# Kernel optimization log

Hardware: AMD Instinct MI355X
Metric: run time of the kernel (lower is better)

The kernel has to match this reference:

```python
import jax, jax.numpy as jnp
import numpy as np

N_NODES = 10000
W_DIM = 512
N_EDGES = 200000


def setup_inputs() -> dict:
    key = jax.random.key(0)
    k1, k2, k3 = jax.random.split(key, 3)
    z_drug = jax.random.normal(k1, (N_NODES, W_DIM), dtype=jnp.float32)
    # glorot-style init for the bilinear weight
    glorot_std = jnp.sqrt(2.0 / (W_DIM + W_DIM)).astype(jnp.float32)
    weight = jax.random.normal(k2, (W_DIM, W_DIM), dtype=jnp.float32) * glorot_std
    batch_edges = jax.random.randint(k3, (2, N_EDGES), 0, N_NODES, dtype=jnp.int64)
    return {"z_drug": z_drug, "weight": weight, "batch_edges": batch_edges}


def reference(z_drug, weight, batch_edges):
    # edge_type == 'drug_drug': both endpoints come from the drug table.
    row_embed = z_drug[batch_edges[0]]  # [E, d]
    col_embed = z_drug[batch_edges[1]]  # [E, d]
    # score_e = row_e @ W @ col_e  == diag((Z1 W) Z2^T) without the N x N blowup
    score = jnp.einsum('ed,df,ef->e', row_embed, weight, col_embed)
    return jax.nn.sigmoid(score)  # is_sigmoid=True default
```

## Files before the change

kernel.cpp:

```cpp
#include <hip/hip_runtime.h>
#include <math.h>

#define DIM     512
#define NNODES  10000
#define NEDGES  200000
#define MPAD    10240
#define NMB     160
#define NGRP    5
#define NB      (NGRP * NNODES)
#define SCAN_N  49
#define GEMM_GRID (NMB * 4)

#define HIST_BLK   50
#define SCAN_BASE  50
#define SCAT_BASE  99
#define SCAT_N     98
#define GEMM_BASE  197
#define FUSE_GRID  (GEMM_BASE + GEMM_GRID)

using floatx4 = __attribute__((ext_vector_type(4))) float;
using half8   = __attribute__((ext_vector_type(8))) _Float16;
using half2v  = __attribute__((ext_vector_type(2))) _Float16;

template <int N> struct IC { static constexpr int v = N; };

__device__ inline float dot2acc(half2v a, half2v b, float c) {
#if __has_builtin(__builtin_amdgcn_fdot2)
    return __builtin_amdgcn_fdot2(a, b, c, false);
#else
    return fmaf((float)a[0], (float)b[0], fmaf((float)a[1], (float)b[1], c));
#endif
}

__device__ inline int aload(const int* p) {
    return __hip_atomic_load(p, __ATOMIC_RELAXED, __HIP_MEMORY_SCOPE_AGENT);
}
__device__ inline void astore(int* p, int v) {
    __hip_atomic_store(p, v, __ATOMIC_RELAXED, __HIP_MEMORY_SCOPE_AGENT);
}
__device__ inline void waitflag(int* f, int target) {
    while (__hip_atomic_load(f, __ATOMIC_RELAXED, __HIP_MEMORY_SCOPE_AGENT) < target)
        __builtin_amdgcn_s_sleep(8);
    __atomic_signal_fence(__ATOMIC_ACQUIRE);
}
__device__ inline void signal(int* f) {
    __atomic_signal_fence(__ATOMIC_RELEASE);
    __hip_atomic_fetch_add(f, 1, __ATOMIC_RELAXED, __HIP_MEMORY_SCOPE_AGENT);
}

#define PREP_ZBLK 2560
__global__ __launch_bounds__(256) void prep(const float* __restrict__ Z,
                                            const float* __restrict__ W,
                                            _Float16* __restrict__ Zh16,
                                            _Float16* __restrict__ Wh16t,
                                            int* __restrict__ counts,
                                            int* __restrict__ flags) {
    const int b = blockIdx.x;
    const int t = threadIdx.x;

    if (b == 0 && t < 4) flags[t] = 0;

    if (b < 196) {
        int i = b * 256 + t;
        if (i < NB) counts[i] = 0;
    }

    if (b < PREP_ZBLK) {
        const int idx8 = (b * 256 + t) * 8;
        const int m = idx8 >> 9;
        float x[8];
        if (m < NNODES) {
            float4 v0 = *(const float4*)(Z + idx8);
            float4 v1 = *(const float4*)(Z + idx8 + 4);
            x[0]=v0.x; x[1]=v0.y; x[2]=v0.z; x[3]=v0.w;
            x[4]=v1.x; x[5]=v1.y; x[6]=v1.z; x[7]=v1.w;
        } else {
            #pragma unroll
            for (int j = 0; j < 8; ++j) x[j] = 0.f;
        }
        half8 h;
        #pragma unroll
        for (int j = 0; j < 8; ++j) h[j] = (_Float16)x[j];
        *(half8*)(Zh16 + idx8) = h;
    } else {
        __shared__ float tile[64][65];
        const int wb = b - PREP_ZBLK;
        const int kb = (wb >> 3) * 64;
        const int nb = (wb & 7) * 64;
        const int kk = t >> 2;
        const int ch = t & 3;

        const float* src = W + (size_t)(kb + kk) * DIM + nb + ch * 16;
        #pragma unroll
        for (int q = 0; q < 4; ++q) {
            float4 v = *(const float4*)(src + q * 4);
            tile[kk][ch * 16 + q * 4 + 0] = v.x;
            tile[kk][ch * 16 + q * 4 + 1] = v.y;
            tile[kk][ch * 16 + q * 4 + 2] = v.z;
            tile[kk][ch * 16 + q * 4 + 3] = v.w;
        }
        __syncthreads();

        const int nn = kk;
        half8 h0, h1;
        #pragma unroll
        for (int i = 0; i < 8; ++i) h0[i] = (_Float16)tile[ch * 16 + i][nn];
        #pragma unroll
        for (int i = 0; i < 8; ++i) h1[i] = (_Float16)tile[ch * 16 + 8 + i][nn];
        _Float16* d = Wh16t + (size_t)(nb + nn) * DIM + kb + ch * 16;
        *(half8*)(d)     = h0;
        *(half8*)(d + 8) = h1;
    }
}

__global__ __launch_bounds__(256, 3) void gemm_sort(
        const _Float16* __restrict__ Zh16,
        const _Float16* __restrict__ Wh16t,
        _Float16* __restrict__ ZWh,
        const int* __restrict__ eidx,
        int* __restrict__ counts,
        int* __restrict__ cursor,
        int* __restrict__ blksum,
        unsigned* __restrict__ keys,
        unsigned short* __restrict__ rows16,
        int* __restrict__ flags)
{
    __shared__ _Float16 Abuf[2][2 * 64 * 32];
    __shared__ _Float16 Bbuf[2][2 * 128 * 32];
    __shared__ int wsum[4];
    __shared__ int sbase;

    const int t   = threadIdx.x;
    const int bid = blockIdx.x;

    if (bid >= GEMM_BASE) {
        const int s8  = bid - GEMM_BASE;
        const int cxd = bid & 7;
        const int rr  = s8 >> 3;
        const int mg  = (rr >> 2) * 8 + cxd;
        const int m0  = mg * 64;
        const int n0  = (rr & 3) * 128;

        const int l  = t & 63;
        const int w  = t >> 6;
        const int wn = w * 32;
        const int lm = l & 15;
        const int lq = l >> 4;
        const unsigned wbase = (unsigned)(t & 192);

        floatx4 acc[4][2] = {};

        auto stage = [&](int buf, int k0) {
            #pragma unroll
            for (int p = 0; p < 2; ++p) {
                const int s   = p * 256 + t;
                const int kk  = s >> 8;
                const int row = (s >> 2) & 63;
                const int ch  = s & 3;
                const _Float16* src = Zh16 + (size_t)(m0 + row) * DIM + k0 + kk * 32 + ch * 8;
                __builtin_amdgcn_global_load_lds(
                    (const __attribute__((address_space(1))) void*)src,
                    (__attribute__((address_space(3))) void*)&Abuf[buf][(p * 256 + wbase) * 8],
                    16, 0, 0);
            }
            #pragma unroll
            for (int p = 0; p < 4; ++p) {
                const int s   = p * 256 + t;
                const int kk  = s >> 9;
                const int row = (s >> 2) & 127;
                const int ch  = s & 3;
                const _Float16* src = Wh16t + (size_t)(n0 + row) * DIM + k0 + kk * 32 + ch * 8;
                __builtin_amdgcn_global_load_lds(
                    (const __attribute__((address_space(1))) void*)src,
                    (__attribute__((address_space(3))) void*)&Bbuf[buf][(p * 256 + wbase) * 8],
                    16, 0, 0);
            }
        };

        stage(0, 0);
        stage(1, 64);

        auto step = [&](auto Sc) {
            constexpr int S   = decltype(Sc)::v;
            constexpr int buf = S & 1;
            if constexpr (S < 7) asm volatile("s_waitcnt vmcnt(6)" ::: "memory");
            else                 asm volatile("s_waitcnt vmcnt(0)" ::: "memory");
            __builtin_amdgcn_sched_barrier(0);
            __builtin_amdgcn_s_barrier();
            __builtin_amdgcn_sched_barrier(0);

            half8 aF[2][4], bF[2][2];
            #pragma unroll
            for (int kk = 0; kk < 2; ++kk) {
                #pragma unroll
                for (int i = 0; i < 4; ++i)
                    aF[kk][i] = *(const half8*)&Abuf[buf][kk * 2048 + (16 * i + lm) * 32 + lq * 8];
                #pragma unroll
                for (int j = 0; j < 2; ++j)
                    bF[kk][j] = *(const half8*)&Bbuf[buf][kk * 4096 + (wn + 16 * j + lm) * 32 + lq * 8];
            }
            asm volatile("s_waitcnt lgkmcnt(0)" ::: "memory");
            __builtin_amdgcn_sched_barrier(0);
            __builtin_amdgcn_s_barrier();
            __builtin_amdgcn_sched_barrier(0);

            if constexpr (S < 6) stage(buf, (S + 2) * 64);

            #pragma unroll
            for (int kk = 0; kk < 2; ++kk)
                #pragma unroll
                for (int i = 0; i < 4; ++i)
                    #pragma unroll
                    for (int j = 0; j < 2; ++j)
                        acc[i][j] = __builtin_amdgcn_mfma_f32_16x16x32_f16(
                            aF[kk][i], bF[kk][j], acc[i][j], 0, 0, 0);
        };

        step(IC<0>{}); step(IC<1>{}); step(IC<2>{}); step(IC<3>{});
        step(IC<4>{}); step(IC<5>{}); step(IC<6>{}); step(IC<7>{});

        #pragma unroll
        for (int i = 0; i < 4; ++i)
            #pragma unroll
            for (int j = 0; j < 2; ++j)
                #pragma unroll
                for (int r = 0; r < 4; ++r) {
                    const int gm = m0 + 16 * i + lq * 4 + r;
                    const int gn = n0 + wn + 16 * j + lm;
                    if (gm < NNODES)
                        ZWh[(size_t)gm * DIM + gn] = (_Float16)acc[i][j][r];
                }
        return;
    }

    if (bid < HIST_BLK) {
        for (int e = bid * 256 + t; e < NEDGES; e += HIST_BLK * 256) {
            int r = eidx[e];
            int c = eidx[NEDGES + e];
            atomicAdd(&counts[(c >> 11) * NNODES + r], 1);
        }
        __syncthreads();
        if (t == 0) signal(&flags[0]);
        return;
    }

    if (bid < SCAT_BASE) {
        const int b = bid - SCAN_BASE;
        const int lane = t & 63;
        const int wv   = t >> 6;

        if (t == 0) waitflag(&flags[0], HIST_BLK);
        __syncthreads();

        const int base = b * 1024 + t * 4;
        int v0 = 0, v1 = 0, v2 = 0, v3 = 0;
        if (base + 3 < NB) {
            v0 = aload(counts + base);
            v1 = aload(counts + base + 1);
            v2 = aload(counts + base + 2);
            v3 = aload(counts + base + 3);
        } else {
            if (base     < NB) v0 = aload(counts + base);
            if (base + 1 < NB) v1 = aload(counts + base + 1);
            if (base + 2 < NB) v2 = aload(counts + base + 2);
        }
        const int ts = v0 + v1 + v2 + v3;
        int incl = ts;
        #pragma unroll
        for (int off = 1; off < 64; off <<= 1) {
            int u = __shfl_up(incl, off, 64);
            if (lane >= off) incl += u;
        }
        if (lane == 63) wsum[wv] = incl;
        __syncthreads();
        int wb = 0;
        #pragma unroll
        for (int k = 0; k < 4; ++k) if (k < wv) wb += wsum[k];
        const int ex   = wb + incl - ts;
        const int pre0 = ex;
        const int pre1 = ex + v0;
        const int pre2 = pre1 + v1;
        const int pre3 = pre2 + v2;
        if (t == 255) astore(blksum + b, wb + incl);
        __syncthreads();
        if (t == 0) { signal(&flags[1]); waitflag(&flags[1], SCAN_N); }
        __syncthreads();

        if (t < 64) {
            int v = (t < b) ? aload(blksum + t) : 0;
            #pragma unroll
            for (int off = 32; off > 0; off >>= 1)
                v += __shfl_xor(v, off, 64);
            if (t == 0) sbase = v;
        }
        __syncthreads();
        const int b0 = sbase;

        if (base + 3 < NB) {
            astore(cursor + base,     b0 + pre0);
            astore(cursor + base + 1, b0 + pre1);
            astore(cursor + base + 2, b0 + pre2);
            astore(cursor + base + 3, b0 + pre3);
        } else {
            if (base     < NB) astore(cursor + base,     b0 + pre0);
            if (base + 1 < NB) astore(cursor + base + 1, b0 + pre1);
            if (base + 2 < NB) astore(cursor + base + 2, b0 + pre2);
        }
        __syncthreads();
        if (t == 0) signal(&flags[2]);
        return;
    }

    {
        if (t == 0) waitflag(&flags[2], SCAN_N);
        __syncthreads();

        for (int e = (bid - SCAT_BASE) * 256 + t; e < NEDGES; e += SCAT_N * 256) {
            int r = eidx[e];
            int c = eidx[NEDGES + e];
            int pos = atomicAdd(&cursor[(c >> 11) * NNODES + r], 1);
            keys[pos]   = ((unsigned)c << 18) | (unsigned)e;
            rows16[pos] = (unsigned short)r;
        }
    }
}

__global__ __launch_bounds__(256) void edge_score_f(const _Float16* __restrict__ ZWh,
                                                    const _Float16* __restrict__ Zh,
                                                    const unsigned* __restrict__ keys,
                                                    const unsigned short* __restrict__ rows16,
                                                    float* __restrict__ out) {
    const int t    = threadIdx.x;
    const int wgid = blockIdx.x * 4 + (t >> 6);
    const int lane = t & 63;
    const int gq   = lane >> 4;
    const int sl   = lane & 15;

    const int ii = wgid * 4 + gq;
    const unsigned k = keys[ii];
    const int c = (int)(k >> 18);
    const int r = (int)rows16[ii];

    const _Float16* rp = ZWh + (size_t)r * DIM + sl * 32;
    const _Float16* cp = Zh  + (size_t)c * DIM + sl * 32;

    half8 ra0 = *(const half8*)(rp);
    half8 ra1 = *(const half8*)(rp + 8);
    half8 ra2 = *(const half8*)(rp + 16);
    half8 ra3 = *(const half8*)(rp + 24);
    half8 c0  = *(const half8*)(cp);
    half8 c1  = *(const half8*)(cp + 8);
    half8 c2  = *(const half8*)(cp + 16);
    half8 c3  = *(const half8*)(cp + 24);

    float s = 0.f;
    #pragma unroll
    for (int d = 0; d < 4; ++d) {
        s = dot2acc((half2v){ra0[2*d], ra0[2*d+1]}, (half2v){c0[2*d], c0[2*d+1]}, s);
        s = dot2acc((half2v){ra1[2*d], ra1[2*d+1]}, (half2v){c1[2*d], c1[2*d+1]}, s);
        s = dot2acc((half2v){ra2[2*d], ra2[2*d+1]}, (half2v){c2[2*d], c2[2*d+1]}, s);
        s = dot2acc((half2v){ra3[2*d], ra3[2*d+1]}, (half2v){c3[2*d], c3[2*d+1]}, s);
    }

    s += __shfl_xor(s, 1, 64);
    s += __shfl_xor(s, 2, 64);
    s += __shfl_xor(s, 4, 64);
    s += __shfl_xor(s, 8, 64);

    if (sl == 0)
        out[k & 0x3FFFFu] = 1.0f / (1.0f + expf(-s));
}

#define GTM 128
#define GTN 64
#define GTK 16
#define LDA 132
#define LDB 68

__global__ __launch_bounds__(256) void gemm_zw(const float* __restrict__ A,
                                               const float* __restrict__ B,
                                               float* __restrict__ C) {
    __shared__ float As[GTK * LDA];
    __shared__ float Bs[GTK * LDB];

    const int t  = threadIdx.x;
    const int m0 = blockIdx.x * GTM;
    const int n0 = blockIdx.y * GTN;
    const int tx = t & 15;
    const int ty = t >> 4;

    float acc[8][4] = {};

    for (int k0 = 0; k0 < DIM; k0 += GTK) {
        #pragma unroll
        for (int p = 0; p < 2; ++p) {
            int f  = t + p * 256;
            int mm = f >> 2;
            int kq = f & 3;
            int m  = m0 + mm;
            float4 v = make_float4(0.f, 0.f, 0.f, 0.f);
            if (m < NNODES)
                v = *(const float4*)(A + (size_t)m * DIM + k0 + kq * 4);
            As[(kq * 4 + 0) * LDA + mm] = v.x;
            As[(kq * 4 + 1) * LDA + mm] = v.y;
            As[(kq * 4 + 2) * LDA + mm] = v.z;
            As[(kq * 4 + 3) * LDA + mm] = v.w;
        }
        {
            int kb = t >> 4, n4 = t & 15;
            *(float4*)&Bs[kb * LDB + n4 * 4] =
                *(const float4*)(B + (size_t)(k0 + kb) * DIM + n0 + n4 * 4);
        }
        __syncthreads();

        #pragma unroll
        for (int kk = 0; kk < GTK; ++kk) {
            float4 a0 = *(const float4*)&As[kk * LDA + ty * 8];
            float4 a1 = *(const float4*)&As[kk * LDA + ty * 8 + 4];
            float4 b  = *(const float4*)&Bs[kk * LDB + tx * 4];
            float av[8] = {a0.x, a0.y, a0.z, a0.w, a1.x, a1.y, a1.z, a1.w};
            float bv[4] = {b.x, b.y, b.z, b.w};
            #pragma unroll
            for (int i = 0; i < 8; ++i)
                #pragma unroll
                for (int j = 0; j < 4; ++j)
                    acc[i][j] = fmaf(av[i], bv[j], acc[i][j]);
        }
        __syncthreads();
    }

    #pragma unroll
    for (int i = 0; i < 8; ++i) {
        int m = m0 + ty * 8 + i;
        if (m < NNODES)
            *(float4*)(C + (size_t)m * DIM + n0 + tx * 4) =
                make_float4(acc[i][0], acc[i][1], acc[i][2], acc[i][3]);
    }
}

__global__ __launch_bounds__(256) void edge_score(const float* __restrict__ ZW,
                                                  const float* __restrict__ Z,
                                                  const int* __restrict__ eidx,
                                                  float* __restrict__ out) {
    const int e    = blockIdx.x * 4 + (threadIdx.x >> 6);
    const int lane = threadIdx.x & 63;

    const int r = eidx[e];
    const int c = eidx[NEDGES + e];

    const float4* pr = (const float4*)(ZW + (size_t)r * DIM);
    const float4* pc = (const float4*)(Z  + (size_t)c * DIM);

    float4 a0 = pr[lane * 2 + 0];
    float4 a1 = pr[lane * 2 + 1];
    float4 b0 = pc[lane * 2 + 0];
    float4 b1 = pc[lane * 2 + 1];

    float s = a0.x * b0.x;
    s = fmaf(a0.y, b0.y, s);
    s = fmaf(a0.z, b0.z, s);
    s = fmaf(a0.w, b0.w, s);
    s = fmaf(a1.x, b1.x, s);
    s = fmaf(a1.y, b1.y, s);
    s = fmaf(a1.z, b1.z, s);
    s = fmaf(a1.w, b1.w, s);

    #pragma unroll
    for (int off = 32; off > 0; off >>= 1)
        s += __shfl_xor(s, off, 64);

    if (lane == 0)
        out[e] = 1.0f / (1.0f + expf(-s));
}

extern "C" void kernel_launch(void* const* d_in, const int* in_sizes, int n_in,
                              void* d_out, int out_size, void* d_ws, size_t ws_size,
                              hipStream_t stream) {
    const float* Z  = (const float*)d_in[0];
    const float* W  = (const float*)d_in[1];
    const int*   EI = (const int*)d_in[2];
    float* out = (float*)d_out;

    char* p = (char*)d_ws;
    _Float16* ZWh   = (_Float16*)p;  p += (size_t)MPAD * DIM * 2;
    _Float16* Zh16  = (_Float16*)p;  p += (size_t)MPAD * DIM * 2;
    _Float16* Wh16t = (_Float16*)p;  p += (size_t)DIM * DIM * 2;
    int* counts  = (int*)p;          p += (size_t)NB * 4;
    int* cursor  = (int*)p;          p += (size_t)NB * 4;
    int* blksum  = (int*)p;          p += (size_t)SCAN_N * 4;
    unsigned* keys = (unsigned*)p;   p += (size_t)NEDGES * 4;
    unsigned short* rows16 = (unsigned short*)p; p += (size_t)NEDGES * 2;
    int* flags = (int*)p;            p += 4 * 4;
    const size_t need_full = (size_t)(p - (char*)d_ws);

    if (ws_size >= need_full) {
        prep<<<PREP_ZBLK + 64, 256, 0, stream>>>(Z, W, Zh16, Wh16t, counts, flags);
        gemm_sort<<<FUSE_GRID, 256, 0, stream>>>(Zh16, Wh16t, ZWh, EI, counts,
                                                 cursor, blksum, keys, rows16, flags);
        edge_score_f<<<NEDGES / 16, 256, 0, stream>>>(ZWh, Zh16, keys, rows16, out);
    } else {
        float* ZW = (float*)d_ws;
        dim3 g1((NNODES + GTM - 1) / GTM, DIM / GTN);
        gemm_zw<<<g1, 256, 0, stream>>>(Z, W, ZW);
        edge_score<<<NEDGES / 4, 256, 0, stream>>>(ZW, Z, EI, out);
    }
}
```

Measured before the change: 135.6 us.

## Move edge histogram into prep kernel, pack sort keys into 64-bit slots

The edge histogram now runs in dedicated blocks of the prep kernel instead of in gemm_sort. The scan blocks no longer wait on a histogram flag, and the freed blocks go to the scatter phase. Counts and flags are zeroed with a memset before prep. Keys and row indices are packed into one 64-bit slot array, so edge_score reads a single load instead of two. This adds a memset launch and atomics inside prep, and the packed slots use more bytes per edge.

```diff
diff --git a/kernel.cpp b/kernel.cpp
--- a/kernel.cpp
+++ b/kernel.cpp
@@ -11,16 +11,15 @@
 #define SCAN_N  49
 #define GEMM_GRID (NMB * 4)
 
-#define HIST_BLK   50
-#define SCAN_BASE  50
-#define SCAT_BASE  99
-#define SCAT_N     98
-#define GEMM_BASE  197
+#define SCAT_BASE  49
+#define SCAT_N     196
+#define GEMM_BASE  245
 #define FUSE_GRID  (GEMM_BASE + GEMM_GRID)
 
 using floatx4 = __attribute__((ext_vector_type(4))) float;
 using half8   = __attribute__((ext_vector_type(8))) _Float16;
 using half2v  = __attribute__((ext_vector_type(2))) _Float16;
+typedef unsigned long long ull;
 
 template <int N> struct IC { static constexpr int v = N; };
 
@@ -49,21 +48,18 @@
 }
 
 #define PREP_ZBLK 2560
+#define PREP_WBASE PREP_ZBLK
+#define PREP_HBASE (PREP_ZBLK + 64)
+#define PREP_HBLK  64
+#define PREP_GRID  (PREP_HBASE + PREP_HBLK)
 __global__ __launch_bounds__(256) void prep(const float* __restrict__ Z,
                                             const float* __restrict__ W,
+                                            const int* __restrict__ eidx,
                                             _Float16* __restrict__ Zh16,
                                             _Float16* __restrict__ Wh16t,
-                                            int* __restrict__ counts,
-                                            int* __restrict__ flags) {
+                                            int* __restrict__ counts) {
     const int b = blockIdx.x;
     const int t = threadIdx.x;
-
-    if (b == 0 && t < 4) flags[t] = 0;
-
-    if (b < 196) {
-        int i = b * 256 + t;
-        if (i < NB) counts[i] = 0;
-    }
 
     if (b < PREP_ZBLK) {
         const int idx8 = (b * 256 + t) * 8;
@@ -82,9 +78,9 @@
         #pragma unroll
         for (int j = 0; j < 8; ++j) h[j] = (_Float16)x[j];
         *(half8*)(Zh16 + idx8) = h;
-    } else {
+    } else if (b < PREP_HBASE) {
         __shared__ float tile[64][65];
-        const int wb = b - PREP_ZBLK;
+        const int wb = b - PREP_WBASE;
         const int kb = (wb >> 3) * 64;
         const int nb = (wb & 7) * 64;
         const int kk = t >> 2;
@@ -110,6 +106,13 @@
         _Float16* d = Wh16t + (size_t)(nb + nn) * DIM + kb + ch * 16;
         *(half8*)(d)     = h0;
         *(half8*)(d + 8) = h1;
+    } else {
+        const int hb = b - PREP_HBASE;
+        for (int e = hb * 256 + t; e < NEDGES; e += PREP_HBLK * 256) {
+            int r = eidx[e];
+            int c = eidx[NEDGES + e];
+            atomicAdd(&counts[(c >> 11) * NNODES + r], 1);
+        }
     }
 }
 
@@ -121,8 +124,7 @@
         int* __restrict__ counts,
         int* __restrict__ cursor,
         int* __restrict__ blksum,
-        unsigned* __restrict__ keys,
-        unsigned short* __restrict__ rows16,
+        ull* __restrict__ slots,
         int* __restrict__ flags)
 {
     __shared__ _Float16 Abuf[2][2 * 64 * 32];
@@ -233,24 +235,10 @@
         return;
     }
 
-    if (bid < HIST_BLK) {
-        for (int e = bid * 256 + t; e < NEDGES; e += HIST_BLK * 256) {
-            int r = eidx[e];
-            int c = eidx[NEDGES + e];
-            atomicAdd(&counts[(c >> 11) * NNODES + r], 1);
-        }
-        __syncthreads();
-        if (t == 0) signal(&flags[0]);
-        return;
-    }
-
     if (bid < SCAT_BASE) {
-        const int b = bid - SCAN_BASE;
+        const int b = bid;
         const int lane = t & 63;
         const int wv   = t >> 6;
-
-        if (t == 0) waitflag(&flags[0], HIST_BLK);
-        __syncthreads();
 
         const int base = b * 1024 + t * 4;
         int v0 = 0, v1 = 0, v2 = 0, v3 = 0;
@@ -319,16 +307,14 @@
             int r = eidx[e];
             int c = eidx[NEDGES + e];
             int pos = atomicAdd(&cursor[(c >> 11) * NNODES + r], 1);
-            keys[pos]   = ((unsigned)c << 18) | (unsigned)e;
-            rows16[pos] = (unsigned short)r;
+            slots[pos] = (ull)(((unsigned)c << 18) | (unsigned)e) | ((ull)(unsigned)r << 32);
         }
     }
 }
 
 __global__ __launch_bounds__(256) void edge_score_f(const _Float16* __restrict__ ZWh,
                                                     const _Float16* __restrict__ Zh,
-                                                    const unsigned* __restrict__ keys,
-                                                    const unsigned short* __restrict__ rows16,
+                                                    const ull* __restrict__ slots,
                                                     float* __restrict__ out) {
     const int t    = threadIdx.x;
     const int wgid = blockIdx.x * 4 + (t >> 6);
@@ -337,9 +323,10 @@
     const int sl   = lane & 15;
 
     const int ii = wgid * 4 + gq;
-    const unsigned k = keys[ii];
+    const ull  v = slots[ii];
+    const unsigned k = (unsigned)v;
     const int c = (int)(k >> 18);
-    const int r = (int)rows16[ii];
+    const int r = (int)((v >> 32) & 0xFFFFu);
 
     const _Float16* rp = ZWh + (size_t)r * DIM + sl * 32;
     const _Float16* cp = Zh  + (size_t)c * DIM + sl * 32;
@@ -486,18 +473,18 @@
     _Float16* Zh16  = (_Float16*)p;  p += (size_t)MPAD * DIM * 2;
     _Float16* Wh16t = (_Float16*)p;  p += (size_t)DIM * DIM * 2;
     int* counts  = (int*)p;          p += (size_t)NB * 4;
+    int* flags   = (int*)p;          p += 4 * 4;
     int* cursor  = (int*)p;          p += (size_t)NB * 4;
     int* blksum  = (int*)p;          p += (size_t)SCAN_N * 4;
-    unsigned* keys = (unsigned*)p;   p += (size_t)NEDGES * 4;
-    unsigned short* rows16 = (unsigned short*)p; p += (size_t)NEDGES * 2;
-    int* flags = (int*)p;            p += 4 * 4;
+    ull* slots   = (ull*)p;          p += (size_t)NEDGES * 8;
     const size_t need_full = (size_t)(p - (char*)d_ws);
 
     if (ws_size >= need_full) {
-        prep<<<PREP_ZBLK + 64, 256, 0, stream>>>(Z, W, Zh16, Wh16t, counts, flags);
+        hipMemsetAsync(counts, 0, (size_t)NB * 4 + 16, stream);
+        prep<<<PREP_GRID, 256, 0, stream>>>(Z, W, EI, Zh16, Wh16t, counts);
         gemm_sort<<<FUSE_GRID, 256, 0, stream>>>(Zh16, Wh16t, ZWh, EI, counts,
-                                                 cursor, blksum, keys, rows16, flags);
-        edge_score_f<<<NEDGES / 16, 256, 0, stream>>>(ZWh, Zh16, keys, rows16, out);
+                                                 cursor, blksum, slots, flags);
+        edge_score_f<<<NEDGES / 16, 256, 0, stream>>>(ZWh, Zh16, slots, out);
     } else {
         float* ZW = (float*)d_ws;
         dim3 g1((NNODES + GTM - 1) / GTM, DIM / GTN);
```

New measurement: 139.8 us. 1.03x slower.
